# Kernel optimization log

Hardware: AMD Instinct MI355X
Metric: run time of the kernel (lower is better)

Reference implementation:

```python
import jax, jax.numpy as jnp
import numpy as np

B, LQ, LK, D, H, DFF = 2, 2048, 2048, 512, 8, 2048


def _xavier(key, shape):
    fan_in, fan_out = shape[0], shape[1]
    lim = float(np.sqrt(6.0 / (fan_in + fan_out)))
    return jax.random.uniform(key, shape, jnp.float32, -lim, lim)


def setup_inputs() -> dict:
    key = jax.random.key(0)
    ks = jax.random.split(key, 8)
    return {
        "inputs": jax.random.normal(ks[0], (B, LQ, D), jnp.float32),
        "encoder_x": jax.random.normal(ks[1], (B, LK, D), jnp.float32),
        "Wq": _xavier(ks[2], (D, D)),
        "Wk": _xavier(ks[3], (D, D)),
        "Wv": _xavier(ks[4], (D, D)),
        "ln1_g": jnp.ones((D,), jnp.float32),
        "ln1_b": jnp.zeros((D,), jnp.float32),
        "W1": jax.random.normal(ks[5], (D, DFF), jnp.float32) * 0.02,
        "b1": jnp.zeros((DFF,), jnp.float32),
        "W2": jax.random.normal(ks[6], (DFF, D), jnp.float32) * 0.02,
        "b2": jnp.zeros((D,), jnp.float32),
        "ln2_g": jnp.ones((D,), jnp.float32),
        "ln2_b": jnp.zeros((D,), jnp.float32),
        "n_heads": H,
    }


def _layer_norm(x, g, b, eps=1e-5):
    mu = jnp.mean(x, axis=-1, keepdims=True)
    var = jnp.var(x, axis=-1, keepdims=True)
    return (x - mu) * jax.lax.rsqrt(var + eps) * g + b


def reference(inputs, encoder_x, Wq, Wk, Wv, ln1_g, ln1_b, W1, b1, W2, b2, ln2_g, ln2_b, n_heads):
    b, lq, d = inputs.shape
    lk = encoder_x.shape[1]
    hd = d // n_heads
    q = (inputs @ Wq).reshape(b, lq, n_heads, hd)
    k = (encoder_x @ Wk).reshape(b, lk, n_heads, hd)
    v = (encoder_x @ Wv).reshape(b, lk, n_heads, hd)
    # scores: [b, h, lq, lk]; scale by sqrt(head_dim) as in source
    scores = jnp.einsum("bqhd,bkhd->bhqk", q, k) / jnp.sqrt(jnp.asarray(hd, q.dtype))
    attn = jax.nn.softmax(scores, axis=-1)
    o = jnp.einsum("bhqk,bkhd->bqhd", attn, v).reshape(b, lq, d)
    out = _layer_norm(o + inputs, ln1_g, ln1_b)
    ff = jax.nn.relu(out @ W1 + b1) @ W2 + b2
    return _layer_norm(ff + out, ln2_g, ln2_b)
```

## Files before the change

### kernel.cpp

```cpp
#include <hip/hip_runtime.h>

typedef __bf16 bf16_t;
typedef __bf16 bf16x8 __attribute__((ext_vector_type(8)));
typedef __bf16 bf16x4 __attribute__((ext_vector_type(4)));
typedef float f32x4 __attribute__((ext_vector_type(4)));
typedef float f32x16 __attribute__((ext_vector_type(16)));
typedef unsigned int u32;
typedef unsigned int u32x2 __attribute__((ext_vector_type(2)));

#define GLB_AS(p) ((const __attribute__((address_space(1))) unsigned int*)(p))
#define LDS_AS(p) ((__attribute__((address_space(3))) unsigned int*)(p))

#define SPLIT_ROWS 32768
#define KLD 68
#define VLD 44

__global__ void cvt_both_kernel(const float* __restrict__ inA, bf16_t* __restrict__ outA, float scaleA,
                                const float* __restrict__ inB, bf16_t* __restrict__ outB)
{
    const int bid = blockIdx.x;
    const float* in;
    bf16_t* out;
    float scale;
    int i;
    if (bid < 2048) { in = inA; out = outA; scale = scaleA; i = (bid * 256 + threadIdx.x) * 4; }
    else            { in = inB; out = outB; scale = 1.0f;  i = ((bid - 2048) * 256 + threadIdx.x) * 4; }
    float4 v = *(const float4*)(in + i);
    bf16x4 o;
    o[0] = (bf16_t)(v.x * scale); o[1] = (bf16_t)(v.y * scale);
    o[2] = (bf16_t)(v.z * scale); o[3] = (bf16_t)(v.w * scale);
    *(bf16x4*)(out + i) = o;
}

__global__ void wtrans_all_kernel(const float* __restrict__ Wq, const float* __restrict__ Wk,
                                  const float* __restrict__ Wv, const float* __restrict__ W1,
                                  const float* __restrict__ W2, bf16_t* __restrict__ Wqkvt,
                                  bf16_t* __restrict__ W1t, bf16_t* __restrict__ W2t)
{
    const int j = blockIdx.x;
    const float* in;
    bf16_t* out;
    int R, C, bx, by;
    if (j < 768) {
        int k = j >> 8, l = j & 255;
        in = (k == 0) ? Wq : (k == 1) ? Wk : Wv;
        out = Wqkvt + k * 512 * 512;
        R = 512; C = 512; bx = l & 15; by = l >> 4;
    } else if (j < 1792) {
        int l = j - 768;
        in = W1; out = W1t; R = 512; C = 2048; bx = l % 64; by = l / 64;
    } else {
        int l = j - 1792;
        in = W2; out = W2t; R = 2048; C = 512; bx = l % 16; by = l / 16;
    }
    __shared__ float tile[32][33];
    const int tid = threadIdx.x;
    const int r0 = by * 32, c0 = bx * 32;
#pragma unroll
    for (int t = 0; t < 4; t++) {
        int r = t * 8 + (tid >> 5), c = tid & 31;
        tile[r][c] = in[(size_t)(r0 + r) * C + c0 + c];
    }
    __syncthreads();
#pragma unroll
    for (int t = 0; t < 4; t++) {
        int c = t * 8 + (tid >> 5), r = tid & 31;
        out[(size_t)(c0 + c) * R + r0 + r] = (bf16_t)tile[r][c];
    }
}

__global__ void vtrans_kernel(const bf16_t* __restrict__ qkv, bf16_t* __restrict__ vt)
{
    __shared__ bf16_t t[64][68];
    const int tid = threadIdx.x;
    const int lk0 = blockIdx.x * 64;
    const int bh = blockIdx.y, b = bh >> 3, h = bh & 7;
#pragma unroll
    for (int j = 0; j < 16; j++) {
        int e = j * 256 + tid;
        int lk_i = e >> 6, d = e & 63;
        t[lk_i][d] = qkv[(size_t)(b * 2048 + lk0 + lk_i) * 1536 + 1024 + h * 64 + d];
    }
    __syncthreads();
#pragma unroll
    for (int j = 0; j < 16; j++) {
        int e = j * 256 + tid;
        int d_i = e >> 6, lk = e & 63;
        vt[((size_t)bh * 64 + d_i) * 2048 + lk0 + lk] = t[lk][d_i];
    }
}

template<int BM, bool SPLITA, bool BIAS, bool RELU, bool OUTBF16>
__global__ __launch_bounds__(256)
void gemm_kernel(const bf16_t* __restrict__ A0, const bf16_t* __restrict__ A1, int nsplit,
                 const bf16_t* __restrict__ Bt, const float* __restrict__ bias,
                 void* __restrict__ Cout, int K, int ldC)
{
    constexpr int FR = BM / 32;
    __shared__ __align__(16) bf16_t As[BM * 32];
    __shared__ __align__(16) bf16_t Bs[128 * 32];
    const int bm = blockIdx.x, bn = blockIdx.y;
    const bf16_t* A = (!SPLITA || bn < nsplit) ? A0 : A1;
    const int tid = threadIdx.x;
    const int lane = tid & 63;
    const int wid = tid >> 6;
    const int wr = wid >> 1, wc = wid & 1;

    f32x4 acc[FR][4] = {};

    const int cb = wid * 2;
    const int lbB0 = cb * 1024 + lane * 16;
    const int rowB0 = lbB0 >> 6, colB0 = (lbB0 & 63) >> 1;
    const int rowB1 = (lbB0 + 1024) >> 6, colB1 = ((lbB0 + 1024) & 63) >> 1;
    const int lbA0 = (BM == 128 ? cb * 1024 : wid * 1024) + lane * 16;
    const int rowA0 = lbA0 >> 6, colA0 = (lbA0 & 63) >> 1;
    const int rowA1 = (lbA0 + 1024) >> 6, colA1 = ((lbA0 + 1024) & 63) >> 1;

    const bf16_t* Abase = A + (size_t)(bm * BM) * K;
    const bf16_t* Bbase = Bt + (size_t)(bn * 128) * K;

    for (int k0 = 0; k0 < K; k0 += 32) {
        if constexpr (BM == 128) {
            __builtin_amdgcn_global_load_lds(GLB_AS(Abase + (size_t)rowA0 * K + k0 + colA0), LDS_AS(As + cb * 512), 16, 0, 0);
            __builtin_amdgcn_global_load_lds(GLB_AS(Abase + (size_t)rowA1 * K + k0 + colA1), LDS_AS(As + cb * 512 + 512), 16, 0, 0);
        } else {
            __builtin_amdgcn_global_load_lds(GLB_AS(Abase + (size_t)rowA0 * K + k0 + colA0), LDS_AS(As + wid * 512), 16, 0, 0);
        }
        __builtin_amdgcn_global_load_lds(GLB_AS(Bbase + (size_t)rowB0 * K + k0 + colB0), LDS_AS(Bs + cb * 512), 16, 0, 0);
        __builtin_amdgcn_global_load_lds(GLB_AS(Bbase + (size_t)rowB1 * K + k0 + colB1), LDS_AS(Bs + cb * 512 + 512), 16, 0, 0);
        __syncthreads();
        bf16x8 af[FR], bfr[4];
#pragma unroll
        for (int f = 0; f < FR; f++)
            af[f] = *(const bf16x8*)&As[(wr * (BM / 2) + f * 16 + (lane & 15)) * 32 + (lane >> 4) * 8];
#pragma unroll
        for (int f = 0; f < 4; f++)
            bfr[f] = *(const bf16x8*)&Bs[(wc * 64 + f * 16 + (lane & 15)) * 32 + (lane >> 4) * 8];
#pragma unroll
        for (int fr = 0; fr < FR; fr++)
#pragma unroll
            for (int fc = 0; fc < 4; fc++)
                acc[fr][fc] = __builtin_amdgcn_mfma_f32_16x16x32_bf16(af[fr], bfr[fc], acc[fr][fc], 0, 0, 0);
        __syncthreads();
    }

    const int rg = (lane >> 4) * 4, cl = lane & 15;
#pragma unroll
    for (int fc = 0; fc < 4; fc++) {
        const int col = bn * 128 + wc * 64 + fc * 16 + cl;
        float bv = 0.f;
        if (BIAS) bv = bias[col];
#pragma unroll
        for (int fr = 0; fr < FR; fr++) {
#pragma unroll
            for (int r = 0; r < 4; r++) {
                int rowg = bm * BM + wr * (BM / 2) + fr * 16 + rg + r;
                float v = acc[fr][fc][r] + bv;
                if (RELU) v = fmaxf(v, 0.f);
                if (OUTBF16) ((bf16_t*)Cout)[(size_t)rowg * ldC + col] = (bf16_t)v;
                else         ((float*)Cout)[(size_t)rowg * ldC + col] = v;
            }
        }
    }
}

union BU { bf16x8 v; u32 d[4]; };

static __device__ __forceinline__ u32 pkbf(float a, float b)
{
    union { bf16_t h[2]; u32 w; } u;
    u.h[0] = (bf16_t)a; u.h[1] = (bf16_t)b;
    return u.w;
}

static __device__ __forceinline__ void plswap(u32 a, u32 b, u32& x, u32& y)
{
#if __has_builtin(__builtin_amdgcn_permlane32_swap)
    u32x2 r = __builtin_amdgcn_permlane32_swap(a, b, false, false);
    x = r[0]; y = r[1];
#else
    const bool hi = (threadIdx.x & 32) != 0;
    u32 sb = __shfl_xor(b, 32), sa = __shfl_xor(a, 32);
    x = hi ? sb : a;
    y = hi ? b : sa;
#endif
}

__global__ __launch_bounds__(256)
void flash_kernel(const bf16_t* __restrict__ QKV, const bf16_t* __restrict__ Vt,
                  bf16_t* __restrict__ Op01, bf16_t* __restrict__ Op23,
                  float2* __restrict__ ml)
{
    const int tid = threadIdx.x, lane = tid & 63, wid = tid >> 6;
    const int bh = blockIdx.y, b = bh >> 3, h = bh & 7;
    const int split = blockIdx.z;
    const int qbase = blockIdx.x * 128 + wid * 32;
    const int l31 = lane & 31, hi = lane >> 5;

    __shared__ __align__(16) bf16_t Kst[2][32 * KLD];
    __shared__ __align__(16) bf16_t Vst[2][64 * VLD];
    __shared__ __align__(16) bf16_t tlds[4][32 * 68];
    bf16_t* tw = &tlds[wid][0];

    const bf16_t* Qp = QKV + (size_t)(b * 2048 + qbase + l31) * 1536 + h * 64 + hi * 8;
    const bf16_t* Kbase = QKV + (size_t)(b * 2048) * 1536 + 512 + h * 64;
    const bf16_t* Vbase = Vt + (size_t)bh * 64 * 2048;

    const int kr = tid >> 3, kc = (tid & 7) * 8;
    const int vr = tid >> 2, vc = (tid & 3) * 8;

    bf16x8 qf[4];
#pragma unroll
    for (int t = 0; t < 4; t++)
        qf[t] = *(const bf16x8*)(Qp + t * 16);

    bf16x8 ones;
#pragma unroll
    for (int e = 0; e < 8; e++) ones[e] = (bf16_t)1.0f;

    f32x16 acc0 = {}, acc1 = {}, accS = {};
    float mrun = -1e30f;

    const int kv0 = split * 512;

    bf16x8 kreg = *(const bf16x8*)(Kbase + (size_t)(kv0 + kr) * 1536 + kc);
    bf16x8 vreg = *(const bf16x8*)(Vbase + (size_t)vr * 2048 + kv0 + vc);
    *(bf16x8*)&Kst[0][kr * KLD + kc] = kreg;
    *(bf16x8*)&Vst[0][vr * VLD + vc] = vreg;
    __syncthreads();

    int buf = 0;
#pragma unroll 2
    for (int kt = kv0; kt < kv0 + 512; kt += 32) {
        const bool nxt = (kt + 32 < kv0 + 512);
        if (nxt) {
            kreg = *(const bf16x8*)(Kbase + (size_t)(kt + 32 + kr) * 1536 + kc);
            vreg = *(const bf16x8*)(Vbase + (size_t)vr * 2048 + kt + 32 + vc);
        }

        bf16x8 kf[4];
#pragma unroll
        for (int t = 0; t < 4; t++)
            kf[t] = *(const bf16x8*)&Kst[buf][l31 * KLD + hi * 8 + t * 16];
        bf16x8 vf00 = *(const bf16x8*)&Vst[buf][l31 * VLD + hi * 8];
        bf16x8 vf01 = *(const bf16x8*)&Vst[buf][l31 * VLD + 16 + hi * 8];
        bf16x8 vf10 = *(const bf16x8*)&Vst[buf][(32 + l31) * VLD + hi * 8];
        bf16x8 vf11 = *(const bf16x8*)&Vst[buf][(32 + l31) * VLD + 16 + hi * 8];

        f32x16 p = {};
        __builtin_amdgcn_s_setprio(1);
        p = __builtin_amdgcn_mfma_f32_32x32x16_bf16(kf[0], qf[0], p, 0, 0, 0);
        p = __builtin_amdgcn_mfma_f32_32x32x16_bf16(kf[1], qf[1], p, 0, 0, 0);
        p = __builtin_amdgcn_mfma_f32_32x32x16_bf16(kf[2], qf[2], p, 0, 0, 0);
        p = __builtin_amdgcn_mfma_f32_32x32x16_bf16(kf[3], qf[3], p, 0, 0, 0);
        __builtin_amdgcn_s_setprio(0);

        float x0 = fmaxf(p[0], p[8]),  x1 = fmaxf(p[1], p[9]);
        float x2 = fmaxf(p[2], p[10]), x3 = fmaxf(p[3], p[11]);
        float x4 = fmaxf(p[4], p[12]), x5 = fmaxf(p[5], p[13]);
        float x6 = fmaxf(p[6], p[14]), x7 = fmaxf(p[7], p[15]);
        x0 = fmaxf(x0, x4); x1 = fmaxf(x1, x5); x2 = fmaxf(x2, x6); x3 = fmaxf(x3, x7);
        float cm = fmaxf(fmaxf(x0, x1), fmaxf(x2, x3));
        {
            u32 r0, r1;
            plswap(__float_as_uint(cm), __float_as_uint(cm), r0, r1);
            cm = fmaxf(__uint_as_float(r0), __uint_as_float(r1));
        }

        if (__any(cm > mrun + 12.0f)) {
            float mnew = fmaxf(mrun, cm);
            float fac = __builtin_amdgcn_exp2f(mrun - mnew);
#pragma unroll
            for (int i = 0; i < 16; i++) { acc0[i] *= fac; acc1[i] *= fac; accS[i] *= fac; }
            mrun = mnew;
        }

        float e[16];
#pragma unroll
        for (int i = 0; i < 16; i++) e[i] = __builtin_amdgcn_exp2f(p[i] - mrun);

        u32 pk0 = pkbf(e[0], e[1]),   pk1 = pkbf(e[2], e[3]);
        u32 pk2 = pkbf(e[4], e[5]),   pk3 = pkbf(e[6], e[7]);
        u32 pk4 = pkbf(e[8], e[9]),   pk5 = pkbf(e[10], e[11]);
        u32 pk6 = pkbf(e[12], e[13]), pk7 = pkbf(e[14], e[15]);
        BU b0, b1;
        plswap(pk0, pk2, b0.d[0], b0.d[2]);
        plswap(pk1, pk3, b0.d[1], b0.d[3]);
        plswap(pk4, pk6, b1.d[0], b1.d[2]);
        plswap(pk5, pk7, b1.d[1], b1.d[3]);

        __builtin_amdgcn_s_setprio(1);
        acc0 = __builtin_amdgcn_mfma_f32_32x32x16_bf16(vf00, b0.v, acc0, 0, 0, 0);
        acc0 = __builtin_amdgcn_mfma_f32_32x32x16_bf16(vf01, b1.v, acc0, 0, 0, 0);
        acc1 = __builtin_amdgcn_mfma_f32_32x32x16_bf16(vf10, b0.v, acc1, 0, 0, 0);
        acc1 = __builtin_amdgcn_mfma_f32_32x32x16_bf16(vf11, b1.v, acc1, 0, 0, 0);
        accS = __builtin_amdgcn_mfma_f32_32x32x16_bf16(ones, b0.v, accS, 0, 0, 0);
        accS = __builtin_amdgcn_mfma_f32_32x32x16_bf16(ones, b1.v, accS, 0, 0, 0);
        __builtin_amdgcn_s_setprio(0);

        if (nxt) {
            *(bf16x8*)&Kst[buf ^ 1][kr * KLD + kc] = kreg;
            *(bf16x8*)&Vst[buf ^ 1][vr * VLD + vc] = vreg;
        }
        __syncthreads();
        buf ^= 1;
    }

    const float lsum = accS[0];
    float inv = 1.f / lsum;
#pragma unroll
    for (int r = 0; r < 16; r++) {
        int drow = (r & 3) + 8 * (r >> 2) + 4 * hi;
        tw[l31 * 68 + drow]      = (bf16_t)(acc0[r] * inv);
        tw[l31 * 68 + 32 + drow] = (bf16_t)(acc1[r] * inv);
    }
    bf16_t* Op = (split < 2) ? Op01 + (size_t)split * SPLIT_ROWS * 64
                             : Op23 + (size_t)(split - 2) * SPLIT_ROWS * 64;
    const size_t rowbase = (size_t)bh * 2048 + qbase;
#pragma unroll
    for (int ps = 0; ps < 4; ps++) {
        int rr = (lane >> 3) + ps * 8;
        int cc = lane & 7;
        bf16x8 ov = *(const bf16x8*)&tw[rr * 68 + cc * 8];
        *(bf16x8*)(Op + (rowbase + rr) * 64 + cc * 8) = ov;
    }
    if (lane < 32)
        ml[(size_t)split * SPLIT_ROWS + rowbase + l31] = make_float2(mrun, lsum);
}

__global__ __launch_bounds__(128)
void combine_ln_kernel(const bf16_t* __restrict__ Op01, const bf16_t* __restrict__ Op23,
                       const float2* __restrict__ ml, const float* __restrict__ resid,
                       const float* __restrict__ g, const float* __restrict__ bta,
                       bf16_t* __restrict__ outb)
{
    const int row = blockIdx.x;
    const int tid = threadIdx.x;
    const int b = row >> 11, q = row & 2047;
    const int d = tid * 4, h = d >> 6, dd = d & 63;
    const size_t prow = ((size_t)(b * 8 + h)) * 2048 + q;

    float2 m0 = ml[prow];
    float2 m1 = ml[SPLIT_ROWS + prow];
    float2 m2 = ml[2 * SPLIT_ROWS + prow];
    float2 m3 = ml[3 * SPLIT_ROWS + prow];
    float M = fmaxf(fmaxf(m0.x, m1.x), fmaxf(m2.x, m3.x));
    float w0 = m0.y * __builtin_amdgcn_exp2f(m0.x - M);
    float w1 = m1.y * __builtin_amdgcn_exp2f(m1.x - M);
    float w2 = m2.y * __builtin_amdgcn_exp2f(m2.x - M);
    float w3 = m3.y * __builtin_amdgcn_exp2f(m3.x - M);
    float winv = 1.f / (w0 + w1 + w2 + w3);

    bf16x4 p0 = *(const bf16x4*)(Op01 + prow * 64 + dd);
    bf16x4 p1 = *(const bf16x4*)(Op01 + (SPLIT_ROWS + prow) * 64 + dd);
    bf16x4 p2 = *(const bf16x4*)(Op23 + prow * 64 + dd);
    bf16x4 p3 = *(const bf16x4*)(Op23 + (SPLIT_ROWS + prow) * 64 + dd);
    float4 rv = ((const float4*)resid)[row * 128 + tid];

    float x0 = (w0 * (float)p0[0] + w1 * (float)p1[0] + w2 * (float)p2[0] + w3 * (float)p3[0]) * winv + rv.x;
    float x1 = (w0 * (float)p0[1] + w1 * (float)p1[1] + w2 * (float)p2[1] + w3 * (float)p3[1]) * winv + rv.y;
    float x2 = (w0 * (float)p0[2] + w1 * (float)p1[2] + w2 * (float)p2[2] + w3 * (float)p3[2]) * winv + rv.z;
    float x3 = (w0 * (float)p0[3] + w1 * (float)p1[3] + w2 * (float)p2[3] + w3 * (float)p3[3]) * winv + rv.w;

    float s = x0 + x1 + x2 + x3;
    float sq = x0 * x0 + x1 * x1 + x2 * x2 + x3 * x3;
#pragma unroll
    for (int dl = 1; dl < 64; dl <<= 1) { s += __shfl_xor(s, dl); sq += __shfl_xor(sq, dl); }
    __shared__ float red[2][2];
    const int wid = tid >> 6;
    if ((tid & 63) == 0) { red[wid][0] = s; red[wid][1] = sq; }
    __syncthreads();
    s = red[0][0] + red[1][0];
    sq = red[0][1] + red[1][1];
    float mu = s * (1.f / 512.f);
    float var = sq * (1.f / 512.f) - mu * mu;
    float rstd = rsqrtf(var + 1e-5f);
    const float4 gv = ((const float4*)g)[tid];
    const float4 bv = ((const float4*)bta)[tid];
    bf16x4 o;
    o[0] = (bf16_t)((x0 - mu) * rstd * gv.x + bv.x);
    o[1] = (bf16_t)((x1 - mu) * rstd * gv.y + bv.y);
    o[2] = (bf16_t)((x2 - mu) * rstd * gv.z + bv.z);
    o[3] = (bf16_t)((x3 - mu) * rstd * gv.w + bv.w);
    *(bf16x4*)(outb + (size_t)row * 512 + tid * 4) = o;
}

template<bool RESBF>
__global__ __launch_bounds__(128)
void add_ln_kernel(const float* __restrict__ a, const void* __restrict__ res,
                   const float* __restrict__ g, const float* __restrict__ bta,
                   float* outf, bf16_t* outb)
{
    const int row = blockIdx.x, tid = threadIdx.x;
    const float4* a4 = (const float4*)(a + (size_t)row * 512);
    float4 av = a4[tid];
    float r0, r1, r2, r3;
    if (RESBF) {
        bf16x4 rv = ((const bf16x4*)res)[row * 128 + tid];
        r0 = (float)rv[0]; r1 = (float)rv[1]; r2 = (float)rv[2]; r3 = (float)rv[3];
    } else {
        float4 rv = ((const float4*)res)[row * 128 + tid];
        r0 = rv.x; r1 = rv.y; r2 = rv.z; r3 = rv.w;
    }
    float x0 = av.x + r0, x1 = av.y + r1, x2 = av.z + r2, x3 = av.w + r3;
    float s = x0 + x1 + x2 + x3;
    float sq = x0 * x0 + x1 * x1 + x2 * x2 + x3 * x3;
#pragma unroll
    for (int d = 1; d < 64; d <<= 1) { s += __shfl_xor(s, d); sq += __shfl_xor(sq, d); }
    __shared__ float red[2][2];
    const int wid = tid >> 6;
    if ((tid & 63) == 0) { red[wid][0] = s; red[wid][1] = sq; }
    __syncthreads();
    s = red[0][0] + red[1][0];
    sq = red[0][1] + red[1][1];
    float mu = s * (1.f / 512.f);
    float var = sq * (1.f / 512.f) - mu * mu;
    float rstd = rsqrtf(var + 1e-5f);
    const float4* g4 = (const float4*)g;
    const float4* b4 = (const float4*)bta;
    float4 gv = g4[tid], bv = b4[tid];
    float4 y;
    y.x = (x0 - mu) * rstd * gv.x + bv.x;
    y.y = (x1 - mu) * rstd * gv.y + bv.y;
    y.z = (x2 - mu) * rstd * gv.z + bv.z;
    y.w = (x3 - mu) * rstd * gv.w + bv.w;
    if (outf) ((float4*)(outf + (size_t)row * 512))[tid] = y;
    if (outb) {
        bf16x4 o;
        o[0] = (bf16_t)y.x; o[1] = (bf16_t)y.y; o[2] = (bf16_t)y.z; o[3] = (bf16_t)y.w;
        *(bf16x4*)(outb + (size_t)row * 512 + tid * 4) = o;
    }
}

extern "C" void kernel_launch(void* const* d_in, const int* in_sizes, int n_in,
                              void* d_out, int out_size, void* d_ws, size_t ws_size,
                              hipStream_t stream)
{
    const float* inputs = (const float*)d_in[0];
    const float* encx   = (const float*)d_in[1];
    const float* Wq     = (const float*)d_in[2];
    const float* Wk     = (const float*)d_in[3];
    const float* Wv     = (const float*)d_in[4];
    const float* ln1g   = (const float*)d_in[5];
    const float* ln1b   = (const float*)d_in[6];
    const float* W1     = (const float*)d_in[7];
    const float* b1     = (const float*)d_in[8];
    const float* W2     = (const float*)d_in[9];
    const float* b2     = (const float*)d_in[10];
    const float* ln2g   = (const float*)d_in[11];
    const float* ln2b   = (const float*)d_in[12];

    char* ws = (char*)d_ws;
    const size_t MB = 1u << 20;
    bf16_t* W1t   = (bf16_t*)(ws);
    bf16_t* W2t   = (bf16_t*)(ws + 2 * MB);
    bf16_t* Xb    = (bf16_t*)(ws + 4 * MB);
    bf16_t* Op01  = (bf16_t*)(ws + 4 * MB);
    bf16_t* Hb    = (bf16_t*)(ws + 4 * MB);
    bf16_t* Eb    = (bf16_t*)(ws + 8 * MB);
    bf16_t* QKVb  = (bf16_t*)(ws + 12 * MB);
    bf16_t* Vtb   = (bf16_t*)(ws + 24 * MB);
    bf16_t* out1b = (bf16_t*)(ws + 24 * MB);
    bf16_t* Wqkvt = (bf16_t*)(ws + 28 * MB);
    float2* mlbuf = (float2*)(ws + 28 * MB);
    bf16_t* Op23  = (bf16_t*)d_out;
    float*  FF    = (float*)d_out;

    cvt_both_kernel<<<4096, 256, 0, stream>>>(inputs, Xb, 0.125f * 1.44269504f, encx, Eb);
    wtrans_all_kernel<<<2816, 256, 0, stream>>>(Wq, Wk, Wv, W1, W2, Wqkvt, W1t, W2t);
    gemm_kernel<64, true, false, false, true><<<dim3(64, 12), 256, 0, stream>>>(
        Xb, Eb, 4, Wqkvt, nullptr, QKVb, 512, 1536);
    vtrans_kernel<<<dim3(32, 16), 256, 0, stream>>>(QKVb, Vtb);
    flash_kernel<<<dim3(16, 16, 4), 256, 0, stream>>>(QKVb, Vtb, Op01, Op23, mlbuf);
    combine_ln_kernel<<<4096, 128, 0, stream>>>(Op01, Op23, mlbuf, inputs, ln1g, ln1b, out1b);
    gemm_kernel<128, false, true, true, true><<<dim3(32, 16), 256, 0, stream>>>(
        out1b, nullptr, 0, W1t, b1, Hb, 512, 2048);
    gemm_kernel<64, false, true, false, false><<<dim3(64, 4), 256, 0, stream>>>(
        Hb, nullptr, 0, W2t, b2, FF, 2048, 512);
    add_ln_kernel<true><<<4096, 128, 0, stream>>>(FF, out1b, ln2g, ln2b, (float*)d_out, nullptr);
}
```

Measured before the change: 135.0 us.

## Shrink flash blocks to two waves, reuse K stage for output, retile QKV GEMM

Flash attention blocks drop from four waves to two, so each covers 64 query rows and the grid doubles. Each thread now loads two K and two V vectors per tile so 128 threads still fill the staging buffers. The separate transpose LDS buffer is removed and the output transpose reuses the K staging area, which lowers shared memory per block and may raise occupancy. The QKV projection GEMM also switches to a 128-wide tile with half as many blocks in x. K/V staging traffic per query row rises because each block serves fewer queries.

```diff
diff --git a/kernel.cpp b/kernel.cpp
--- a/kernel.cpp
+++ b/kernel.cpp
@@ -186,7 +186,7 @@
 #endif
 }
 
-__global__ __launch_bounds__(256)
+__global__ __launch_bounds__(128)
 void flash_kernel(const bf16_t* __restrict__ QKV, const bf16_t* __restrict__ Vt,
                   bf16_t* __restrict__ Op01, bf16_t* __restrict__ Op23,
                   float2* __restrict__ ml)
@@ -194,13 +194,11 @@
     const int tid = threadIdx.x, lane = tid & 63, wid = tid >> 6;
     const int bh = blockIdx.y, b = bh >> 3, h = bh & 7;
     const int split = blockIdx.z;
-    const int qbase = blockIdx.x * 128 + wid * 32;
+    const int qbase = blockIdx.x * 64 + wid * 32;
     const int l31 = lane & 31, hi = lane >> 5;
 
     __shared__ __align__(16) bf16_t Kst[2][32 * KLD];
     __shared__ __align__(16) bf16_t Vst[2][64 * VLD];
-    __shared__ __align__(16) bf16_t tlds[4][32 * 68];
-    bf16_t* tw = &tlds[wid][0];
 
     const bf16_t* Qp = QKV + (size_t)(b * 2048 + qbase + l31) * 1536 + h * 64 + hi * 8;
     const bf16_t* Kbase = QKV + (size_t)(b * 2048) * 1536 + 512 + h * 64;
@@ -223,10 +221,14 @@
 
     const int kv0 = split * 512;
 
-    bf16x8 kreg = *(const bf16x8*)(Kbase + (size_t)(kv0 + kr) * 1536 + kc);
-    bf16x8 vreg = *(const bf16x8*)(Vbase + (size_t)vr * 2048 + kv0 + vc);
-    *(bf16x8*)&Kst[0][kr * KLD + kc] = kreg;
-    *(bf16x8*)&Vst[0][vr * VLD + vc] = vreg;
+    bf16x8 kreg0 = *(const bf16x8*)(Kbase + (size_t)(kv0 + kr) * 1536 + kc);
+    bf16x8 kreg1 = *(const bf16x8*)(Kbase + (size_t)(kv0 + 16 + kr) * 1536 + kc);
+    bf16x8 vreg0 = *(const bf16x8*)(Vbase + (size_t)vr * 2048 + kv0 + vc);
+    bf16x8 vreg1 = *(const bf16x8*)(Vbase + (size_t)(32 + vr) * 2048 + kv0 + vc);
+    *(bf16x8*)&Kst[0][kr * KLD + kc] = kreg0;
+    *(bf16x8*)&Kst[0][(16 + kr) * KLD + kc] = kreg1;
+    *(bf16x8*)&Vst[0][vr * VLD + vc] = vreg0;
+    *(bf16x8*)&Vst[0][(32 + vr) * VLD + vc] = vreg1;
     __syncthreads();
 
     int buf = 0;
@@ -234,8 +236,10 @@
     for (int kt = kv0; kt < kv0 + 512; kt += 32) {
         const bool nxt = (kt + 32 < kv0 + 512);
         if (nxt) {
-            kreg = *(const bf16x8*)(Kbase + (size_t)(kt + 32 + kr) * 1536 + kc);
-            vreg = *(const bf16x8*)(Vbase + (size_t)vr * 2048 + kt + 32 + vc);
+            kreg0 = *(const bf16x8*)(Kbase + (size_t)(kt + 32 + kr) * 1536 + kc);
+            kreg1 = *(const bf16x8*)(Kbase + (size_t)(kt + 48 + kr) * 1536 + kc);
+            vreg0 = *(const bf16x8*)(Vbase + (size_t)vr * 2048 + kt + 32 + vc);
+            vreg1 = *(const bf16x8*)(Vbase + (size_t)(32 + vr) * 2048 + kt + 32 + vc);
         }
 
         bf16x8 kf[4];
@@ -299,8 +303,10 @@
         __builtin_amdgcn_s_setprio(0);
 
         if (nxt) {
-            *(bf16x8*)&Kst[buf ^ 1][kr * KLD + kc] = kreg;
-            *(bf16x8*)&Vst[buf ^ 1][vr * VLD + vc] = vreg;
+            *(bf16x8*)&Kst[buf ^ 1][kr * KLD + kc] = kreg0;
+            *(bf16x8*)&Kst[buf ^ 1][(16 + kr) * KLD + kc] = kreg1;
+            *(bf16x8*)&Vst[buf ^ 1][vr * VLD + vc] = vreg0;
+            *(bf16x8*)&Vst[buf ^ 1][(32 + vr) * VLD + vc] = vreg1;
         }
         __syncthreads();
         buf ^= 1;
@@ -308,11 +314,12 @@
 
     const float lsum = accS[0];
     float inv = 1.f / lsum;
+    bf16_t* tw = (bf16_t*)Kst + wid * (32 * KLD);
 #pragma unroll
     for (int r = 0; r < 16; r++) {
         int drow = (r & 3) + 8 * (r >> 2) + 4 * hi;
-        tw[l31 * 68 + drow]      = (bf16_t)(acc0[r] * inv);
-        tw[l31 * 68 + 32 + drow] = (bf16_t)(acc1[r] * inv);
+        tw[l31 * KLD + drow]      = (bf16_t)(acc0[r] * inv);
+        tw[l31 * KLD + 32 + drow] = (bf16_t)(acc1[r] * inv);
     }
     bf16_t* Op = (split < 2) ? Op01 + (size_t)split * SPLIT_ROWS * 64
                              : Op23 + (size_t)(split - 2) * SPLIT_ROWS * 64;
@@ -321,7 +328,7 @@
     for (int ps = 0; ps < 4; ps++) {
         int rr = (lane >> 3) + ps * 8;
         int cc = lane & 7;
-        bf16x8 ov = *(const bf16x8*)&tw[rr * 68 + cc * 8];
+        bf16x8 ov = *(const bf16x8*)&tw[rr * KLD + cc * 8];
         *(bf16x8*)(Op + (rowbase + rr) * 64 + cc * 8) = ov;
     }
     if (lane < 32)
@@ -468,10 +475,10 @@
 
     cvt_both_kernel<<<4096, 256, 0, stream>>>(inputs, Xb, 0.125f * 1.44269504f, encx, Eb);
     wtrans_all_kernel<<<2816, 256, 0, stream>>>(Wq, Wk, Wv, W1, W2, Wqkvt, W1t, W2t);
-    gemm_kernel<64, true, false, false, true><<<dim3(64, 12), 256, 0, stream>>>(
+    gemm_kernel<128, true, false, false, true><<<dim3(32, 12), 256, 0, stream>>>(
         Xb, Eb, 4, Wqkvt, nullptr, QKVb, 512, 1536);
     vtrans_kernel<<<dim3(32, 16), 256, 0, stream>>>(QKVb, Vtb);
-    flash_kernel<<<dim3(16, 16, 4), 256, 0, stream>>>(QKVb, Vtb, Op01, Op23, mlbuf);
+    flash_kernel<<<dim3(32, 16, 4), 128, 0, stream>>>(QKVb, Vtb, Op01, Op23, mlbuf);
     combine_ln_kernel<<<4096, 128, 0, stream>>>(Op01, Op23, mlbuf, inputs, ln1g, ln1b, out1b);
     gemm_kernel<128, false, true, true, true><<<dim3(32, 16), 256, 0, stream>>>(
         out1b, nullptr, 0, W1t, b1, Hb, 512, 2048);
```

Result: slower. 145.6 us (+7.8%).
